# Performance work log

Measured on AMD Instinct MI355X. Metric: run time of the kernel, lower is better.

The kernel has to match this reference:

```python
import jax, jax.numpy as jnp
import numpy as np

# Problem sizes (match input_specs)
B, D, N, M, C = 2, 128, 131072, 131072, 128
IGNORE = -1  # config.data.ignore_label


def setup_inputs() -> dict:
    key = jax.random.key(0)
    k1, k2, k3, k4, k5 = jax.random.split(key, 5)
    vb = jax.random.randint(k1, (N, 1), 0, B)
    vxyz = jax.random.randint(k2, (N, 3), 0, D)
    coords = jnp.concatenate([vb, vxyz], axis=1).astype(jnp.int32)  # (N,4) [b,x,y,z]
    qb = jax.random.randint(k3, (M, 1), 0, B).astype(jnp.float32)
    qxyz = jax.random.uniform(k4, (M, 3), minval=0.0, maxval=float(D - 1))
    query_points = jnp.concatenate([qb, qxyz], axis=1)  # (M,4) [b,x,y,z]
    features = jax.random.normal(k5, (N, C), dtype=jnp.float32)  # (N,C)
    return {"coords": coords, "features": features, "query_points": query_points}


def reference(coords, features, query_points):
    n_vox = coords.shape[0]
    b = coords[:, 0]
    xyz = coords[:, 1:]
    # per-batch coordinate shift (torch.amin per batch), scale_factor == 1
    shift = jax.ops.segment_min(xyz, b, num_segments=B)  # (B,3)
    xyz = xyz - shift[b]
    qb = query_points[:, 0].astype(jnp.int32)
    q = query_points[:, 1:] - shift[qb].astype(query_points.dtype)  # (M,3)

    # dense occupancy: voxel index at occupied cells, IGNORE elsewhere
    occ = jnp.full((B, D, D, D), IGNORE, dtype=jnp.int32)
    occ = occ.at[b, xyz[:, 0], xyz[:, 1], xyz[:, 2]].set(
        jnp.arange(n_vox, dtype=jnp.int32))

    # 8-corner trilinear gather
    q0 = jnp.floor(q)
    f = q - q0                              # fractional part, (M,3)
    q0i = q0.astype(jnp.int32)
    offs = jnp.array([[i, j, k] for i in (0, 1) for j in (0, 1) for k in (0, 1)],
                     dtype=jnp.int32)       # (8,3)
    corner = q0i[:, None, :] + offs[None]   # (M,8,3)
    inb = jnp.all((corner >= 0) & (corner < D), axis=-1)  # (M,8)
    cc = jnp.clip(corner, 0, D - 1)
    idx = occ[qb[:, None], cc[..., 0], cc[..., 1], cc[..., 2]]  # (M,8)

    # trilinear weights: prod over dims of f (corner==1) or 1-f (corner==0)
    w = jnp.prod(jnp.where(offs[None].astype(bool), f[:, None, :], 1.0 - f[:, None, :]),
                 axis=-1)                   # (M,8)
    valid = inb & (idx >= 0)
    wv = jnp.where(valid, w, 0.0)
    wsum = wv.sum(-1)                       # (M,)

    safe_idx = jnp.clip(idx, 0, None)
    gathered = features[safe_idx]           # (M,8,C)
    query_features = jnp.einsum('mk,mkc->mc', wv, gathered) / \
        jnp.maximum(wsum, 1e-8)[:, None]    # normalized by valid weight mass

    interpolation_indices = jnp.where(valid, idx, IGNORE)
    accum_voxel_weights = jax.ops.segment_sum(
        wv.reshape(-1), safe_idx.reshape(-1), num_segments=n_vox)
    return query_features, interpolation_indices, wv, accum_voxel_weights
```

## Files before the change

### kernel.cpp

```cpp
#include <hip/hip_runtime.h>
#include <limits.h>

#define NBATCH 2
#define DIM 128
#define NVOX 131072
#define NQ 131072
#define NC 128
#define OCC_SIZE (NBATCH * DIM * DIM * DIM)

#define QF_OFF  0
#define IDX_OFF (NQ * NC)
#define WV_OFF  (IDX_OFF + NQ * 8)
#define ACC_OFF (WV_OFF + NQ * 8)

__global__ void k_init(int* __restrict__ occ, int* __restrict__ shift,
                       float* __restrict__ accum) {
    int tid = blockIdx.x * blockDim.x + threadIdx.x;
    int stride = gridDim.x * blockDim.x;
    if (tid < 6) shift[tid] = INT_MAX;
    for (int j = tid; j < NVOX; j += stride) accum[j] = 0.f;
    int4* occ4 = (int4*)occ;
    int4 neg1 = make_int4(-1, -1, -1, -1);
    for (int j = tid; j < OCC_SIZE / 4; j += stride) occ4[j] = neg1;
}

#define SHIFT_BLOCKS 64
__global__ __launch_bounds__(256) void k_shift(const int* __restrict__ coords,
                                               int* __restrict__ shift) {
    __shared__ int sm[4][6];
    int tid = blockIdx.x * blockDim.x + threadIdx.x;
    int stride = gridDim.x * blockDim.x;
    int m0 = INT_MAX, m1 = INT_MAX, m2 = INT_MAX;
    int m3 = INT_MAX, m4 = INT_MAX, m5 = INT_MAX;
    const int4* c4 = (const int4*)coords;
    for (int i = tid; i < NVOX; i += stride) {
        int4 c = c4[i];
        if (c.x == 0) { m0 = min(m0, c.y); m1 = min(m1, c.z); m2 = min(m2, c.w); }
        else          { m3 = min(m3, c.y); m4 = min(m4, c.z); m5 = min(m5, c.w); }
    }
#define WREDUCE(mv)                                           \
    _Pragma("unroll")                                         \
    for (int off = 32; off >= 1; off >>= 1)                   \
        mv = min(mv, __shfl_xor(mv, off, 64));
    WREDUCE(m0) WREDUCE(m1) WREDUCE(m2)
    WREDUCE(m3) WREDUCE(m4) WREDUCE(m5)
#undef WREDUCE
    int wave = threadIdx.x >> 6;
    if ((threadIdx.x & 63) == 0) {
        sm[wave][0] = m0; sm[wave][1] = m1; sm[wave][2] = m2;
        sm[wave][3] = m3; sm[wave][4] = m4; sm[wave][5] = m5;
    }
    __syncthreads();
    if (threadIdx.x == 0) {
        m0 = min(min(sm[0][0], sm[1][0]), min(sm[2][0], sm[3][0]));
        m1 = min(min(sm[0][1], sm[1][1]), min(sm[2][1], sm[3][1]));
        m2 = min(min(sm[0][2], sm[1][2]), min(sm[2][2], sm[3][2]));
        m3 = min(min(sm[0][3], sm[1][3]), min(sm[2][3], sm[3][3]));
        m4 = min(min(sm[0][4], sm[1][4]), min(sm[2][4], sm[3][4]));
        m5 = min(min(sm[0][5], sm[1][5]), min(sm[2][5], sm[3][5]));
        atomicMin(&shift[0], m0); atomicMin(&shift[1], m1); atomicMin(&shift[2], m2);
        atomicMin(&shift[3], m3); atomicMin(&shift[4], m4); atomicMin(&shift[5], m5);
    }
}

__global__ void k_build(const int* __restrict__ coords, const int* __restrict__ shift,
                        int* __restrict__ occ) {
    int i = blockIdx.x * blockDim.x + threadIdx.x;
    if (i >= NVOX) return;
    int4 c = ((const int4*)coords)[i];
    int b = c.x;
    int x = c.y - shift[b * 3 + 0];
    int y = c.z - shift[b * 3 + 1];
    int z = c.w - shift[b * 3 + 2];
    atomicMax(&occ[((b * DIM + x) * DIM + y) * DIM + z], i);
}

__global__ __launch_bounds__(256) void k_query(
    const float* __restrict__ qpts, const float* __restrict__ feats,
    const int* __restrict__ occ, const int* __restrict__ shift,
    float* __restrict__ out) {
    int lane = threadIdx.x & 63;
    int gwave = blockIdx.x * 4 + (threadIdx.x >> 6);
    int qbase = gwave * 8;

    int qi = lane >> 3, k = lane & 7;
    int q = qbase + qi;
    float4 qp = ((const float4*)qpts)[q];
    int qb = (int)qp.x;
    float qx = qp.y - (float)shift[qb * 3 + 0];
    float qy = qp.z - (float)shift[qb * 3 + 1];
    float qz = qp.w - (float)shift[qb * 3 + 2];
    float fx0 = floorf(qx), fy0 = floorf(qy), fz0 = floorf(qz);
    float fx = qx - fx0, fy = qy - fy0, fz = qz - fz0;
    int ox = (k >> 2) & 1, oy = (k >> 1) & 1, oz = k & 1;
    int cx = (int)fx0 + ox, cy = (int)fy0 + oy, cz = (int)fz0 + oz;
    bool inb = ((unsigned)cx < DIM) && ((unsigned)cy < DIM) && ((unsigned)cz < DIM);
    int ccx = min(max(cx, 0), DIM - 1);
    int ccy = min(max(cy, 0), DIM - 1);
    int ccz = min(max(cz, 0), DIM - 1);
    int idx = occ[((qb * DIM + ccx) * DIM + ccy) * DIM + ccz];
    float w = (ox ? fx : 1.f - fx) * (oy ? fy : 1.f - fy) * (oz ? fz : 1.f - fz);
    bool valid = inb && (idx >= 0);
    float wvk = valid ? w : 0.f;

    out[IDX_OFF + (size_t)qbase * 8 + lane] = valid ? (float)idx : -1.f;
    out[WV_OFF  + (size_t)qbase * 8 + lane] = wvk;
    if (valid && wvk != 0.f) atomicAdd(out + ACC_OFF + idx, wvk);

    float wsum = wvk;
    wsum += __shfl_xor(wsum, 1, 64);
    wsum += __shfl_xor(wsum, 2, 64);
    wsum += __shfl_xor(wsum, 4, 64);

    int sidx = valid ? idx : 0;
    unsigned long long vm = __ballot(wvk != 0.f);
    const float2* f2 = (const float2*)feats;
    float2 acc[8];
#pragma unroll
    for (int g = 0; g < 8; ++g) { acc[g].x = 0.f; acc[g].y = 0.f; }
#pragma unroll
    for (int g = 0; g < 8; ++g) {
        unsigned int sub = (unsigned int)(vm >> (g * 8)) & 0xffu;
        while (sub) {
            int j = __ffs(sub) - 1; sub &= sub - 1;
            int src = g * 8 + j;
            float wv_j = __shfl(wvk, src, 64);
            int   idx_j = __shfl(sidx, src, 64);
            float2 fv = f2[(size_t)idx_j * 64 + lane];
            acc[g].x = fmaf(wv_j, fv.x, acc[g].x);
            acc[g].y = fmaf(wv_j, fv.y, acc[g].y);
        }
    }

    float2* qf = (float2*)(out + QF_OFF);
#pragma unroll
    for (int g = 0; g < 8; ++g) {
        float ws = __shfl(wsum, g * 8, 64);
        float denom = fmaxf(ws, 1e-8f);
        float2 r;
        r.x = acc[g].x / denom;
        r.y = acc[g].y / denom;
        qf[(size_t)(qbase + g) * 64 + lane] = r;
    }
}

extern "C" void kernel_launch(void* const* d_in, const int* in_sizes, int n_in,
                              void* d_out, int out_size, void* d_ws, size_t ws_size,
                              hipStream_t stream) {
    const int*   coords = (const int*)d_in[0];
    const float* feats  = (const float*)d_in[1];
    const float* qpts   = (const float*)d_in[2];
    float* out = (float*)d_out;

    int* shift = (int*)d_ws;
    int* occ   = (int*)((char*)d_ws + 256);

    k_init<<<2048, 256, 0, stream>>>(occ, shift, out + ACC_OFF);
    k_shift<<<SHIFT_BLOCKS, 256, 0, stream>>>(coords, shift);
    k_build<<<(NVOX + 255) / 256, 256, 0, stream>>>(coords, shift, occ);
    k_query<<<NQ / 32, 256, 0, stream>>>(qpts, feats, occ, shift, out);
}
```

Measured before the change: 51.02 us.

## Fuse init and shift reduction into one kernel with per-block partial minima

```diff
diff --git a/kernel.cpp b/kernel.cpp
--- a/kernel.cpp
+++ b/kernel.cpp
@@ -5,80 +5,95 @@
 #define DIM 128
 #define NVOX 131072
 #define NQ 131072
-#define NC 128
 #define OCC_SIZE (NBATCH * DIM * DIM * DIM)
 
 #define QF_OFF  0
-#define IDX_OFF (NQ * NC)
+#define IDX_OFF (NQ * 128)
 #define WV_OFF  (IDX_OFF + NQ * 8)
 #define ACC_OFF (WV_OFF + NQ * 8)
 
-__global__ void k_init(int* __restrict__ occ, int* __restrict__ shift,
-                       float* __restrict__ accum) {
-    int tid = blockIdx.x * blockDim.x + threadIdx.x;
-    int stride = gridDim.x * blockDim.x;
-    if (tid < 6) shift[tid] = INT_MAX;
+#define SHIFT_BLOCKS 64
+
+#define WREDUCE_MIN(mv)                                       \
+    _Pragma("unroll")                                         \
+    for (int off = 32; off >= 1; off >>= 1)                   \
+        mv = min(mv, __shfl_xor(mv, off, 64));
+
+__global__ __launch_bounds__(256) void k_prep(const int* __restrict__ coords,
+                                              int* __restrict__ sp,
+                                              int* __restrict__ occ,
+                                              float* __restrict__ accum) {
+    int tid = blockIdx.x * 256 + threadIdx.x;
+    int stride = gridDim.x * 256;
     for (int j = tid; j < NVOX; j += stride) accum[j] = 0.f;
     int4* occ4 = (int4*)occ;
     int4 neg1 = make_int4(-1, -1, -1, -1);
     for (int j = tid; j < OCC_SIZE / 4; j += stride) occ4[j] = neg1;
-}
 
-#define SHIFT_BLOCKS 64
-__global__ __launch_bounds__(256) void k_shift(const int* __restrict__ coords,
-                                               int* __restrict__ shift) {
-    __shared__ int sm[4][6];
-    int tid = blockIdx.x * blockDim.x + threadIdx.x;
-    int stride = gridDim.x * blockDim.x;
-    int m0 = INT_MAX, m1 = INT_MAX, m2 = INT_MAX;
-    int m3 = INT_MAX, m4 = INT_MAX, m5 = INT_MAX;
-    const int4* c4 = (const int4*)coords;
-    for (int i = tid; i < NVOX; i += stride) {
-        int4 c = c4[i];
-        if (c.x == 0) { m0 = min(m0, c.y); m1 = min(m1, c.z); m2 = min(m2, c.w); }
-        else          { m3 = min(m3, c.y); m4 = min(m4, c.z); m5 = min(m5, c.w); }
-    }
-#define WREDUCE(mv)                                           \
-    _Pragma("unroll")                                         \
-    for (int off = 32; off >= 1; off >>= 1)                   \
-        mv = min(mv, __shfl_xor(mv, off, 64));
-    WREDUCE(m0) WREDUCE(m1) WREDUCE(m2)
-    WREDUCE(m3) WREDUCE(m4) WREDUCE(m5)
-#undef WREDUCE
-    int wave = threadIdx.x >> 6;
-    if ((threadIdx.x & 63) == 0) {
-        sm[wave][0] = m0; sm[wave][1] = m1; sm[wave][2] = m2;
-        sm[wave][3] = m3; sm[wave][4] = m4; sm[wave][5] = m5;
-    }
-    __syncthreads();
-    if (threadIdx.x == 0) {
-        m0 = min(min(sm[0][0], sm[1][0]), min(sm[2][0], sm[3][0]));
-        m1 = min(min(sm[0][1], sm[1][1]), min(sm[2][1], sm[3][1]));
-        m2 = min(min(sm[0][2], sm[1][2]), min(sm[2][2], sm[3][2]));
-        m3 = min(min(sm[0][3], sm[1][3]), min(sm[2][3], sm[3][3]));
-        m4 = min(min(sm[0][4], sm[1][4]), min(sm[2][4], sm[3][4]));
-        m5 = min(min(sm[0][5], sm[1][5]), min(sm[2][5], sm[3][5]));
-        atomicMin(&shift[0], m0); atomicMin(&shift[1], m1); atomicMin(&shift[2], m2);
-        atomicMin(&shift[3], m3); atomicMin(&shift[4], m4); atomicMin(&shift[5], m5);
+    if (blockIdx.x < SHIFT_BLOCKS) {
+        __shared__ int sm[4][6];
+        int i0 = blockIdx.x * 256 + threadIdx.x;
+        int sstride = SHIFT_BLOCKS * 256;
+        int m0 = INT_MAX, m1 = INT_MAX, m2 = INT_MAX;
+        int m3 = INT_MAX, m4 = INT_MAX, m5 = INT_MAX;
+        const int4* c4 = (const int4*)coords;
+        for (int i = i0; i < NVOX; i += sstride) {
+            int4 c = c4[i];
+            if (c.x == 0) { m0 = min(m0, c.y); m1 = min(m1, c.z); m2 = min(m2, c.w); }
+            else          { m3 = min(m3, c.y); m4 = min(m4, c.z); m5 = min(m5, c.w); }
+        }
+        WREDUCE_MIN(m0) WREDUCE_MIN(m1) WREDUCE_MIN(m2)
+        WREDUCE_MIN(m3) WREDUCE_MIN(m4) WREDUCE_MIN(m5)
+        int wave = threadIdx.x >> 6;
+        if ((threadIdx.x & 63) == 0) {
+            sm[wave][0] = m0; sm[wave][1] = m1; sm[wave][2] = m2;
+            sm[wave][3] = m3; sm[wave][4] = m4; sm[wave][5] = m5;
+        }
+        __syncthreads();
+        if (threadIdx.x == 0) {
+            #pragma unroll
+            for (int c = 0; c < 6; ++c) {
+                int v = min(min(sm[0][c], sm[1][c]), min(sm[2][c], sm[3][c]));
+                sp[c * SHIFT_BLOCKS + blockIdx.x] = v;
+            }
+        }
     }
 }
 
-__global__ void k_build(const int* __restrict__ coords, const int* __restrict__ shift,
-                        int* __restrict__ occ) {
-    int i = blockIdx.x * blockDim.x + threadIdx.x;
-    if (i >= NVOX) return;
+__device__ __forceinline__ void load_shift(const int* __restrict__ sp, int* sh) {
+    if (threadIdx.x < 64) {
+        int l = threadIdx.x;
+        #pragma unroll
+        for (int c = 0; c < 6; ++c) {
+            int v = sp[c * SHIFT_BLOCKS + l];
+            WREDUCE_MIN(v)
+            if (l == 0) sh[c] = v;
+        }
+    }
+    __syncthreads();
+}
+
+__global__ __launch_bounds__(256) void k_build(const int* __restrict__ coords,
+                                               const int* __restrict__ sp,
+                                               int* __restrict__ occ) {
+    __shared__ int sh[6];
+    load_shift(sp, sh);
+    int i = blockIdx.x * 256 + threadIdx.x;
     int4 c = ((const int4*)coords)[i];
     int b = c.x;
-    int x = c.y - shift[b * 3 + 0];
-    int y = c.z - shift[b * 3 + 1];
-    int z = c.w - shift[b * 3 + 2];
+    int x = c.y - sh[b * 3 + 0];
+    int y = c.z - sh[b * 3 + 1];
+    int z = c.w - sh[b * 3 + 2];
     atomicMax(&occ[((b * DIM + x) * DIM + y) * DIM + z], i);
 }
 
 __global__ __launch_bounds__(256) void k_query(
     const float* __restrict__ qpts, const float* __restrict__ feats,
-    const int* __restrict__ occ, const int* __restrict__ shift,
+    const int* __restrict__ occ, const int* __restrict__ sp,
     float* __restrict__ out) {
+    __shared__ int sh[6];
+    load_shift(sp, sh);
+
     int lane = threadIdx.x & 63;
     int gwave = blockIdx.x * 4 + (threadIdx.x >> 6);
     int qbase = gwave * 8;
@@ -87,9 +102,9 @@
     int q = qbase + qi;
     float4 qp = ((const float4*)qpts)[q];
     int qb = (int)qp.x;
-    float qx = qp.y - (float)shift[qb * 3 + 0];
-    float qy = qp.z - (float)shift[qb * 3 + 1];
-    float qz = qp.w - (float)shift[qb * 3 + 2];
+    float qx = qp.y - (float)sh[qb * 3 + 0];
+    float qy = qp.z - (float)sh[qb * 3 + 1];
+    float qz = qp.w - (float)sh[qb * 3 + 2];
     float fx0 = floorf(qx), fy0 = floorf(qy), fz0 = floorf(qz);
     float fx = qx - fx0, fy = qy - fy0, fz = qz - fz0;
     int ox = (k >> 2) & 1, oy = (k >> 1) & 1, oz = k & 1;
@@ -111,6 +126,7 @@
     wsum += __shfl_xor(wsum, 1, 64);
     wsum += __shfl_xor(wsum, 2, 64);
     wsum += __shfl_xor(wsum, 4, 64);
+    float inv = __builtin_amdgcn_rcpf(fmaxf(wsum, 1e-8f));
 
     int sidx = valid ? idx : 0;
     unsigned long long vm = __ballot(wvk != 0.f);
@@ -135,11 +151,10 @@
     float2* qf = (float2*)(out + QF_OFF);
 #pragma unroll
     for (int g = 0; g < 8; ++g) {
-        float ws = __shfl(wsum, g * 8, 64);
-        float denom = fmaxf(ws, 1e-8f);
+        float iv = __shfl(inv, g * 8, 64);
         float2 r;
-        r.x = acc[g].x / denom;
-        r.y = acc[g].y / denom;
+        r.x = acc[g].x * iv;
+        r.y = acc[g].y * iv;
         qf[(size_t)(qbase + g) * 64 + lane] = r;
     }
 }
@@ -152,11 +167,10 @@
     const float* qpts   = (const float*)d_in[2];
     float* out = (float*)d_out;
 
-    int* shift = (int*)d_ws;
-    int* occ   = (int*)((char*)d_ws + 256);
+    int* sp  = (int*)d_ws;
+    int* occ = (int*)((char*)d_ws + 4096);
 
-    k_init<<<2048, 256, 0, stream>>>(occ, shift, out + ACC_OFF);
-    k_shift<<<SHIFT_BLOCKS, 256, 0, stream>>>(coords, shift);
-    k_build<<<(NVOX + 255) / 256, 256, 0, stream>>>(coords, shift, occ);
-    k_query<<<NQ / 32, 256, 0, stream>>>(qpts, feats, occ, shift, out);
+    k_prep<<<2048, 256, 0, stream>>>(coords, sp, occ, out + ACC_OFF);
+    k_build<<<NVOX / 256, 256, 0, stream>>>(coords, sp, occ);
+    k_query<<<NQ / 32, 256, 0, stream>>>(qpts, feats, occ, sp, out);
 }
```

Result: faster. 49.37 us (-3.2%).
